# Performance work log

Measured on AMD Instinct MI355X. Metric: run time of the kernel, lower is better.

## Reference

```python
import jax, jax.numpy as jnp
import numpy as np

D = 64            # node_out_feats
G = 1000          # number of graphs in batch
NPG = 32          # nodes per graph
N = G * NPG       # total nodes = 32000
E = 80000         # total edges
NODE_IN = 74
EDGE_IN = 12
EH = 128          # edge_hidden_feats
STEPS_MP = 6
STEPS_S2S = 6
LSTM_LAYERS = 3
N_TASKS = 1


def setup_inputs() -> dict:
    key = jax.random.key(0)
    ks = jax.random.split(key, 32)

    def lin(k, fi, fo):
        return (jax.random.normal(k, (fi, fo), jnp.float32) / np.float32(np.sqrt(fi)))

    # edges constrained within graphs
    eg = jax.random.randint(ks[0], (E,), 0, G)
    inp = {
        "node_feats": jax.random.normal(ks[1], (N, NODE_IN), jnp.float32),
        "edge_feats": jax.random.normal(ks[2], (E, EDGE_IN), jnp.float32),
        "src": (eg * NPG + jax.random.randint(ks[3], (E,), 0, NPG)).astype(jnp.int32),
        "dst": (eg * NPG + jax.random.randint(ks[4], (E,), 0, NPG)).astype(jnp.int32),
        "segment_ids": (jnp.arange(N, dtype=jnp.int32) // NPG),
        "Wp": lin(ks[5], NODE_IN, D), "bp": jnp.zeros((D,), jnp.float32),
        "We1": lin(ks[6], EDGE_IN, EH), "be1": jnp.zeros((EH,), jnp.float32),
        "We2": lin(ks[7], EH, D * D), "be2": jnp.zeros((D * D,), jnp.float32),
        "b_conv": jnp.zeros((D,), jnp.float32),
        "gru_Wx": lin(ks[8], D, 3 * D), "gru_Wh": lin(ks[9], D, 3 * D),
        "gru_bx": jnp.zeros((3 * D,), jnp.float32), "gru_bh": jnp.zeros((3 * D,), jnp.float32),
        "Wout1": lin(ks[10], 2 * D, D), "bout1": jnp.zeros((D,), jnp.float32),
        "Wout2": lin(ks[11], D, N_TASKS), "bout2": jnp.zeros((N_TASKS,), jnp.float32),
    }
    for l in range(LSTM_LAYERS):
        fi = 2 * D if l == 0 else D
        inp[f"lstm_Wx{l}"] = lin(ks[12 + 4 * l], fi, 4 * D)
        inp[f"lstm_Wh{l}"] = lin(ks[13 + 4 * l], D, 4 * D)
        inp[f"lstm_bx{l}"] = jnp.zeros((4 * D,), jnp.float32)
        inp[f"lstm_bh{l}"] = jnp.zeros((4 * D,), jnp.float32)
    return inp


def reference(node_feats, edge_feats, src, dst, segment_ids,
              Wp, bp, We1, be1, We2, be2, b_conv,
              gru_Wx, gru_Wh, gru_bx, gru_bh,
              Wout1, bout1, Wout2, bout2,
              lstm_Wx0, lstm_Wh0, lstm_bx0, lstm_bh0,
              lstm_Wx1, lstm_Wh1, lstm_bx1, lstm_bh1,
              lstm_Wx2, lstm_Wh2, lstm_bx2, lstm_bh2):
    # ---- MPNNGNN ----
    h = jax.nn.relu(node_feats @ Wp + bp)                 # [N, D]
    hidden = h                                            # GRU hidden state
    # edge network -> per-edge [D, D] weight matrix (edge feats are constant,
    # so compute once; DGL recomputes each step with identical result)
    W_edge = (jax.nn.relu(edge_feats @ We1 + be1) @ We2 + be2).reshape(E, D, D)
    for _ in range(STEPS_MP):
        msg = jnp.einsum('ed,edo->eo', h[src], W_edge)    # [E, D] per-edge matvec
        agg = jax.ops.segment_sum(msg, dst, num_segments=N) + b_conv
        x = jax.nn.relu(agg)
        # GRU cell (torch gate order r, z, n)
        gx = x @ gru_Wx + gru_bx
        gh = hidden @ gru_Wh + gru_bh
        r = jax.nn.sigmoid(gx[:, :D] + gh[:, :D])
        z = jax.nn.sigmoid(gx[:, D:2 * D] + gh[:, D:2 * D])
        n = jnp.tanh(gx[:, 2 * D:] + r * gh[:, 2 * D:])
        hidden = (1.0 - z) * n + z * hidden
        h = hidden
    # ---- Set2Set readout ----
    lstm = [(lstm_Wx0, lstm_Wh0, lstm_bx0, lstm_bh0),
            (lstm_Wx1, lstm_Wh1, lstm_bx1, lstm_bh1),
            (lstm_Wx2, lstm_Wh2, lstm_bx2, lstm_bh2)]
    hs = [jnp.zeros((G, D), h.dtype) for _ in range(LSTM_LAYERS)]
    cs = [jnp.zeros((G, D), h.dtype) for _ in range(LSTM_LAYERS)]
    q_star = jnp.zeros((G, 2 * D), h.dtype)
    for _ in range(STEPS_S2S):
        xq = q_star
        for l, (Wx, Wh, bx, bh) in enumerate(lstm):
            gates = xq @ Wx + bx + hs[l] @ Wh + bh        # [G, 4D], torch order i,f,g,o
            i, f, g_, o = jnp.split(gates, 4, axis=-1)
            c = jax.nn.sigmoid(f) * cs[l] + jax.nn.sigmoid(i) * jnp.tanh(g_)
            hs[l] = jax.nn.sigmoid(o) * jnp.tanh(c)
            cs[l] = c
            xq = hs[l]
        q = xq                                            # [G, D]
        e = jnp.sum(h * q[segment_ids], axis=-1)          # [N] attention logits
        emax = jax.ops.segment_max(e, segment_ids, num_segments=G)
        ee = jnp.exp(e - emax[segment_ids])
        alpha = ee / jax.ops.segment_sum(ee, segment_ids, num_segments=G)[segment_ids]
        readout = jax.ops.segment_sum(h * alpha[:, None], segment_ids, num_segments=G)
        q_star = jnp.concatenate([q, readout], axis=-1)   # [G, 2D]
    # ---- prediction head ----
    pred = jax.nn.relu(q_star @ Wout1 + bout1) @ Wout2 + bout2
    return pred, q_star
```

## Files before the change

kernel.cpp:

```cpp
#include <hip/hip_runtime.h>

typedef __attribute__((ext_vector_type(8))) _Float16 f16x8;
typedef __attribute__((ext_vector_type(2))) _Float16 f16x2;
typedef __attribute__((ext_vector_type(4))) float floatx4;

union HFrag { uint4 u4; f16x8 v; unsigned short s[8]; };
union HS { _Float16 h; unsigned short u; };
union UH2 { unsigned int u; f16x2 h; };

__device__ __forceinline__ float bf2f(unsigned short u) {
  return __uint_as_float(((unsigned int)u) << 16);
}
__device__ __forceinline__ float h2f(unsigned short u) { HS z; z.u = u; return (float)z.h; }
__device__ __forceinline__ unsigned short f2h(float f) { HS z; z.h = (_Float16)f; return z.u; }
__device__ __forceinline__ float sigmf(float x) { return 1.0f / (1.0f + expf(-x)); }

__device__ __forceinline__ float ldi(const void* p, long i, bool f32) {
  return f32 ? ((const float*)p)[i] : bf2f(((const unsigned short*)p)[i]);
}

__device__ __forceinline__ void dma16(unsigned short* lds, const unsigned short* g) {
  __builtin_amdgcn_global_load_lds(
      (const __attribute__((address_space(1))) unsigned int*)g,
      (__attribute__((address_space(3))) unsigned int*)lds,
      16, 0, 0);
}

#define WAIT_VM4()   __builtin_amdgcn_s_waitcnt(0x0F74)
#define WAIT_VM0()   __builtin_amdgcn_s_waitcnt(0x0F70)
#define WAIT_LGKM0() __builtin_amdgcn_s_waitcnt(0xC07F)

#define SAFE_BARRIER() do {                      \
  __builtin_amdgcn_sched_barrier(0);             \
  WAIT_LGKM0();                                  \
  __builtin_amdgcn_s_barrier();                  \
  __builtin_amdgcn_sched_barrier(0);             \
} while (0)

#define NNODES 32000
#define NEDGES 80000
#define NGRAPH 1000

#define MFMA_F16 __builtin_amdgcn_mfma_f32_16x16x32_f16

__global__ __launch_bounds__(256) void detect_kernel(
    const unsigned short* __restrict__ nf, int* __restrict__ flag) {
  __shared__ float sm[256];
  float m = 0.f;
  for (int i = threadIdx.x; i < 4096; i += 256) {
    float v = fabsf(bf2f(nf[i]));
    if (isfinite(v)) m = fmaxf(m, v);
    else m = 1e30f;
  }
  sm[threadIdx.x] = m;
  __syncthreads();
  if (threadIdx.x == 0) {
    float mm = 0.f;
    for (int i = 0; i < 256; ++i) mm = fmaxf(mm, sm[i]);
    flag[0] = (mm > 1e6f) ? 1 : 0;
  }
}

__global__ __launch_bounds__(256) void prep_kernel(
    const int* __restrict__ dflag,
    const void* __restrict__ Wx, const void* __restrict__ Wh,
    const void* __restrict__ bx, const void* __restrict__ bh,
    const void* __restrict__ bconv,
    unsigned short* __restrict__ WxH, unsigned short* __restrict__ WhH,
    float* __restrict__ bxf, float* __restrict__ bhf, float* __restrict__ bconvf) {
  bool f32 = dflag[0] != 0;
  int idx = blockIdx.x * 256 + threadIdx.x;
  int j = idx >> 6, k = idx & 63;
  WxH[idx] = f2h(ldi(Wx, k * 192 + j, f32));
  WhH[idx] = f2h(ldi(Wh, k * 192 + j, f32));
  if (idx < 192) { bxf[idx] = ldi(bx, idx, f32); bhf[idx] = ldi(bh, idx, f32); }
  if (idx < 64) bconvf[idx] = ldi(bconv, idx, f32);
}

__global__ __launch_bounds__(256) void lstmprep_kernel(
    const int* __restrict__ dflag,
    const void* Wx0, const void* Wh0, const void* bx0, const void* bh0,
    const void* Wx1, const void* Wh1, const void* bx1, const void* bh1,
    const void* Wx2, const void* Wh2, const void* bx2, const void* bh2,
    float4* __restrict__ LW, float* __restrict__ bsum) {
  bool f32 = dflag[0] != 0;
  int idx = blockIdx.x * 256 + threadIdx.x;
  int l, base, fi;
  if (idx < 12288)      { l = 0; base = 0;     fi = 128; }
  else if (idx < 20480) { l = 1; base = 12288; fi = 64; }
  else                  { l = 2; base = 20480; fi = 64; }
  const void* Wx = (l == 0) ? Wx0 : (l == 1) ? Wx1 : Wx2;
  const void* Wh = (l == 0) ? Wh0 : (l == 1) ? Wh1 : Wh2;
  int r = idx - base;
  int c = r >> 8, t = r & 255;
  float v[4];
#pragma unroll
  for (int i2 = 0; i2 < 4; ++i2) {
    int k = c * 4 + i2;
    v[i2] = (k < fi) ? ldi(Wx, (long)k * 256 + t, f32)
                     : ldi(Wh, (long)(k - fi) * 256 + t, f32);
  }
  float4 o; o.x = v[0]; o.y = v[1]; o.z = v[2]; o.w = v[3];
  LW[idx] = o;
  if (idx < 768) {
    int ll = idx >> 8, j = idx & 255;
    const void* bx = (ll == 0) ? bx0 : (ll == 1) ? bx1 : bx2;
    const void* bh = (ll == 0) ? bh0 : (ll == 1) ? bh1 : bh2;
    bsum[idx] = ldi(bx, j, f32) + ldi(bh, j, f32);
  }
}

__global__ __launch_bounds__(256) void nodeproj_kernel(
    const int* __restrict__ dflag,
    const void* __restrict__ nf, const void* __restrict__ Wp,
    const void* __restrict__ bp, float* __restrict__ hstate) {
  bool f32 = dflag[0] != 0;
  int lane = threadIdx.x & 63;
  int n = blockIdx.x * 4 + (threadIdx.x >> 6);
  float acc = ldi(bp, lane, f32);
  for (int k = 0; k < 74; ++k)
    acc += ldi(nf, (long)n * 74 + k, f32) * ldi(Wp, k * 64 + lane, f32);
  hstate[n * 64 + lane] = fmaxf(acc, 0.0f);
}

__global__ __launch_bounds__(256) void we2t_kernel(
    const int* __restrict__ dflag,
    const void* __restrict__ We2, unsigned short* __restrict__ We2T) {
  bool f32 = dflag[0] != 0;
  int idx = blockIdx.x * 256 + threadIdx.x;
  int j = idx & 7;
  int gs = (idx >> 3) & 7;
  int o = (idx >> 6) & 63;
  int k = idx >> 12;
  int g = gs ^ (o & 7);
  int d = g * 8 + j;
  We2T[idx] = f2h(ldi(We2, (long)k * 4096 + d * 64 + o, f32));
}

__global__ __launch_bounds__(256) void be2t_kernel(
    const int* __restrict__ dflag,
    const void* __restrict__ be2, unsigned short* __restrict__ be2T) {
  bool f32 = dflag[0] != 0;
  int idx = blockIdx.x * 256 + threadIdx.x;
  int j = idx & 7;
  int gs = (idx >> 3) & 7;
  int o = idx >> 6;
  int g = gs ^ (o & 7);
  int d = g * 8 + j;
  be2T[idx] = f2h(ldi(be2, (long)d * 64 + o, f32));
}

__global__ __launch_bounds__(256) void count_kernel(
    const int* __restrict__ dst, int* __restrict__ cnt) {
  int e = blockIdx.x * 256 + threadIdx.x;
  if (e < NEDGES) atomicAdd(&cnt[dst[e]], 1);
}

__global__ __launch_bounds__(256) void scan_kernel(
    const int* __restrict__ cnt, int* __restrict__ row_ptr, int* __restrict__ cur) {
  __shared__ int part[256];
  int t = threadIdx.x;
  int base = t * 125;
  int s = 0;
  for (int i = 0; i < 125; ++i) s += cnt[base + i];
  part[t] = s;
  __syncthreads();
  if (t == 0) {
    int run = 0;
    for (int i = 0; i < 256; ++i) { int v = part[i]; part[i] = run; run += v; }
  }
  __syncthreads();
  int run = part[t];
  for (int i = 0; i < 125; ++i) {
    row_ptr[base + i] = run;
    cur[base + i] = run;
    run += cnt[base + i];
  }
  if (t == 255) row_ptr[32000] = run;
}

__global__ __launch_bounds__(256) void fill_kernel(
    const int* __restrict__ dst, int* __restrict__ cur, int* __restrict__ eidx) {
  int e = blockIdx.x * 256 + threadIdx.x;
  if (e < NEDGES) { int p = atomicAdd(&cur[dst[e]], 1); eidx[p] = e; }
}

__global__ __launch_bounds__(256, 2) void msg_z_kernel(
    const int* __restrict__ dflag,
    const float* __restrict__ hstate,
    const void* __restrict__ ef, const void* __restrict__ We1,
    const void* __restrict__ be1,
    const unsigned short* __restrict__ We2T,
    const unsigned short* __restrict__ be2T,
    const int* __restrict__ src, const int* __restrict__ eidx,
    const int* __restrict__ row_ptr,
    float* __restrict__ msgbuf) {
  bool f32 = dflag[0] != 0;
  __shared__ __align__(16) unsigned short BtL[2][8192];
  __shared__ __align__(16) unsigned int Zs[2][64][68];
  __shared__ float we1T_s[1536];
  __shared__ float be1_s[128];

  int t = threadIdx.x, lane = t & 63, w = t >> 6;
  int c16 = lane & 15, q = lane >> 4;
  int nb = blockIdx.x * 64;
  int p0 = row_ptr[nb], p1 = row_ptr[nb + 64];
  int nE = p1 - p0;
  if (nE <= 0) return;

  for (int i = t; i < 1536; i += 256) {
    int k = i / 12, j = i - k * 12;
    we1T_s[i] = ldi(We1, j * 128 + k, f32);
  }
  if (t < 128) be1_s[t] = ldi(be1, t, f32);

  HFrag bhi[4][2], blo[4][2];
#pragma unroll
  for (int nt = 0; nt < 4; ++nt)
#pragma unroll
    for (int ks = 0; ks < 2; ++ks) {
      const float* hp = hstate + (size_t)(nb + nt * 16 + c16) * 64 + ks * 32 + q * 8;
      float4 v0 = *(const float4*)hp;
      float4 v1 = *(const float4*)(hp + 4);
      float vv[8] = {v0.x, v0.y, v0.z, v0.w, v1.x, v1.y, v1.z, v1.w};
#pragma unroll
      for (int j = 0; j < 8; ++j) {
        HS hi; hi.h = (_Float16)vv[j];
        bhi[nt][ks].s[j] = hi.u;
        blo[nt][ks].s[j] = f2h(vv[j] - (float)hi.h);
      }
    }
  __syncthreads();

  int arow = (w * 16 + c16) * 64;
  int g0q = (q ^ (c16 & 7)) * 8;
  int g1q = ((4 + q) ^ (c16 & 7)) * 8;

  for (int et = 0; et < nE; et += 256) {
    if (et > 0) SAFE_BARRIER();
    int me = et + t;
    bool act = me < nE;
    int pos = p0 + (act ? me : 0);
    int eg = eidx[pos];
    int r = src[eg] - nb;
    float efr[12];
#pragma unroll
    for (int j = 0; j < 12; ++j) efr[j] = ldi(ef, (long)eg * 12 + j, f32);

    dma16(&BtL[0][0] + w * 1024, be2T + w * 1024 + lane * 8);
    dma16(&BtL[0][0] + w * 1024 + 512, be2T + w * 1024 + 512 + lane * 8);
    dma16(&BtL[1][0] + w * 1024, We2T + w * 1024 + lane * 8);
    dma16(&BtL[1][0] + w * 1024 + 512, We2T + w * 1024 + 512 + lane * 8);
    dma16(&BtL[1][0] + 4096 + w * 1024, We2T + 4096 + w * 1024 + lane * 8);
    dma16(&BtL[1][0] + 4096 + w * 1024 + 512, We2T + 4096 + w * 1024 + 512 + lane * 8);
    WAIT_VM0();

    floatx4 hacc[4];
#pragma unroll
    for (int nt = 0; nt < 4; ++nt) hacc[nt] = (floatx4){0.f, 0.f, 0.f, 0.f};
    {
      HFrag aB0, aB1;
      aB0.u4 = *(const uint4*)&BtL[0][arow + g0q];
      aB1.u4 = *(const uint4*)&BtL[0][arow + g1q];
#pragma unroll
      for (int nt = 0; nt < 4; ++nt) {
        hacc[nt] = MFMA_F16(aB0.v, bhi[nt][0].v, hacc[nt], 0, 0, 0);
        hacc[nt] = MFMA_F16(aB0.v, blo[nt][0].v, hacc[nt], 0, 0, 0);
        hacc[nt] = MFMA_F16(aB1.v, bhi[nt][1].v, hacc[nt], 0, 0, 0);
        hacc[nt] = MFMA_F16(aB1.v, blo[nt][1].v, hacc[nt], 0, 0, 0);
      }
    }
    __builtin_amdgcn_sched_barrier(0);
    WAIT_LGKM0();
    __builtin_amdgcn_sched_barrier(0);
    dma16(&BtL[0][0] + w * 1024, We2T + 8192 + w * 1024 + lane * 8);
    dma16(&BtL[0][0] + w * 1024 + 512, We2T + 8192 + w * 1024 + 512 + lane * 8);
    dma16(&BtL[0][0] + 4096 + w * 1024, We2T + 12288 + w * 1024 + lane * 8);
    dma16(&BtL[0][0] + 4096 + w * 1024 + 512, We2T + 12288 + w * 1024 + 512 + lane * 8);
#pragma unroll
    for (int nt = 0; nt < 4; ++nt)
      *(floatx4*)&Zs[1][nt * 16 + c16][w * 16 + q * 4] = hacc[nt];
    SAFE_BARRIER();

    floatx4 msgv[16];
    if (act) {
#pragma unroll
      for (int og = 0; og < 16; ++og)
        msgv[og] = *(const floatx4*)&Zs[1][r][og * 4];
    }

    for (int c = 0; c < 64; ++c) {
      int cb = (c + 1) & 1;
      int zc = c & 1;
      if (c == 63) WAIT_VM0(); else WAIT_VM4();
      HFrag a00, a01, a10, a11;
      a00.u4 = *(const uint4*)&BtL[cb][arow + g0q];
      a01.u4 = *(const uint4*)&BtL[cb][arow + g1q];
      a10.u4 = *(const uint4*)&BtL[cb][4096 + arow + g0q];
      a11.u4 = *(const uint4*)&BtL[cb][4096 + arow + g1q];
      __builtin_amdgcn_sched_barrier(0);
      WAIT_LGKM0();
      __builtin_amdgcn_sched_barrier(0);
      if (c + 2 < 64) {
        const unsigned short* G = We2T + (size_t)(c + 2) * 8192 + w * 1024 + lane * 8;
        unsigned short* L = &BtL[cb][0] + w * 1024;
        dma16(L, G); dma16(L + 512, G + 512);
        dma16(L + 4096, G + 4096); dma16(L + 4096 + 512, G + 4096 + 512);
      }
      floatx4 z0[4], z1[4];
#pragma unroll
      for (int nt = 0; nt < 4; ++nt) {
        z0[nt] = (floatx4){0.f, 0.f, 0.f, 0.f};
        z1[nt] = (floatx4){0.f, 0.f, 0.f, 0.f};
      }
#pragma unroll
      for (int nt = 0; nt < 4; ++nt) {
        z0[nt] = MFMA_F16(a00.v, bhi[nt][0].v, z0[nt], 0, 0, 0);
        z0[nt] = MFMA_F16(a00.v, blo[nt][0].v, z0[nt], 0, 0, 0);
        z0[nt] = MFMA_F16(a01.v, bhi[nt][1].v, z0[nt], 0, 0, 0);
        z0[nt] = MFMA_F16(a01.v, blo[nt][1].v, z0[nt], 0, 0, 0);
        z1[nt] = MFMA_F16(a10.v, bhi[nt][0].v, z1[nt], 0, 0, 0);
        z1[nt] = MFMA_F16(a10.v, blo[nt][0].v, z1[nt], 0, 0, 0);
        z1[nt] = MFMA_F16(a11.v, bhi[nt][1].v, z1[nt], 0, 0, 0);
        z1[nt] = MFMA_F16(a11.v, blo[nt][1].v, z1[nt], 0, 0, 0);
      }
#pragma unroll
      for (int nt = 0; nt < 4; ++nt) {
        uint4 st;
        HS p0h, p1h;
        p0h.h = (_Float16)z0[nt][0]; p1h.h = (_Float16)z1[nt][0];
        st.x = (unsigned int)p0h.u | ((unsigned int)p1h.u << 16);
        p0h.h = (_Float16)z0[nt][1]; p1h.h = (_Float16)z1[nt][1];
        st.y = (unsigned int)p0h.u | ((unsigned int)p1h.u << 16);
        p0h.h = (_Float16)z0[nt][2]; p1h.h = (_Float16)z1[nt][2];
        st.z = (unsigned int)p0h.u | ((unsigned int)p1h.u << 16);
        p0h.h = (_Float16)z0[nt][3]; p1h.h = (_Float16)z1[nt][3];
        st.w = (unsigned int)p0h.u | ((unsigned int)p1h.u << 16);
        *(uint4*)&Zs[zc][nt * 16 + c16][w * 16 + q * 4] = st;
      }
      SAFE_BARRIER();

      if (act) {
        int k0 = c * 2;
        float u0 = be1_s[k0], u1 = be1_s[k0 + 1];
#pragma unroll
        for (int j = 0; j < 12; ++j) {
          u0 += efr[j] * we1T_s[k0 * 12 + j];
          u1 += efr[j] * we1T_s[(k0 + 1) * 12 + j];
        }
        u0 = fmaxf(u0, 0.f); u1 = fmaxf(u1, 0.f);
        HS ua, ub; ua.h = (_Float16)u0; ub.h = (_Float16)u1;
        UH2 uu; uu.u = (unsigned int)ua.u | ((unsigned int)ub.u << 16);
#pragma unroll
        for (int og = 0; og < 16; ++og) {
          uint4 zz = *(const uint4*)&Zs[zc][r][og * 4];
          UH2 a;
          a.u = zz.x; msgv[og][0] = __builtin_amdgcn_fdot2(a.h, uu.h, msgv[og][0], false);
          a.u = zz.y; msgv[og][1] = __builtin_amdgcn_fdot2(a.h, uu.h, msgv[og][1], false);
          a.u = zz.z; msgv[og][2] = __builtin_amdgcn_fdot2(a.h, uu.h, msgv[og][2], false);
          a.u = zz.w; msgv[og][3] = __builtin_amdgcn_fdot2(a.h, uu.h, msgv[og][3], false);
        }
      }
    }

    if (act) {
      float* mp = msgbuf + (size_t)pos * 64;
#pragma unroll
      for (int og = 0; og < 16; ++og) *(floatx4*)(mp + og * 4) = msgv[og];
    }
  }
}

__global__ __launch_bounds__(256, 2) void gru_kernel(
    float* __restrict__ hstate, const float* __restrict__ msgbuf,
    const int* __restrict__ row_ptr,
    const unsigned short* __restrict__ WxH, const unsigned short* __restrict__ WhH,
    const float* __restrict__ bxf, const float* __restrict__ bhf,
    const float* __restrict__ bconvf) {
  __shared__ __align__(16) unsigned short Xhi[64][72];
  __shared__ __align__(16) unsigned short Xlo[64][72];
  __shared__ __align__(16) unsigned short Hh[64][72];
  __shared__ unsigned short SRZ[128][68];
  __shared__ float GXn[64][66];
  __shared__ float GHn[64][66];
  int t = threadIdx.x;
  int nb = blockIdx.x * 64;

#pragma unroll
  for (int i = 0; i < 16; ++i) {
    int idx = t + i * 256;
    int n = idx >> 6, c = idx & 63;
    int node = nb + n;
    float a = bconvf[c];
    int p0 = row_ptr[node], p1 = row_ptr[node + 1];
    for (int p = p0; p < p1; ++p) a += msgbuf[(size_t)p * 64 + c];
    a = fmaxf(a, 0.f);
    HS hi; hi.h = (_Float16)a;
    Xhi[n][c] = hi.u;
    Xlo[n][c] = f2h(a - (float)hi.h);
    Hh[n][c] = f2h(hstate[(size_t)node * 64 + c]);
  }
  __syncthreads();

  int lane = t & 63, w = t >> 6;
  int c16 = lane & 15, q = lane >> 4;
  floatx4 gx[3][4], gh[3][4];
#pragma unroll
  for (int jt = 0; jt < 3; ++jt)
#pragma unroll
    for (int nt = 0; nt < 4; ++nt) {
      gx[jt][nt] = (floatx4){0.f, 0.f, 0.f, 0.f};
      gh[jt][nt] = (floatx4){0.f, 0.f, 0.f, 0.f};
    }
#pragma unroll
  for (int kc = 0; kc < 2; ++kc) {
    int kof = kc * 32 + q * 8;
    HFrag ax[3], ah[3];
#pragma unroll
    for (int jt = 0; jt < 3; ++jt) {
      long off = (long)((w * 3 + jt) * 16 + c16) * 64 + kof;
      ax[jt].u4 = *(const uint4*)(WxH + off);
      ah[jt].u4 = *(const uint4*)(WhH + off);
    }
    HFrag bxh[4], bxl[4], bhf_[4];
#pragma unroll
    for (int nt = 0; nt < 4; ++nt) {
      int n = nt * 16 + c16;
      bxh[nt].u4 = *(const uint4*)&Xhi[n][kof];
      bxl[nt].u4 = *(const uint4*)&Xlo[n][kof];
      bhf_[nt].u4 = *(const uint4*)&Hh[n][kof];
    }
#pragma unroll
    for (int jt = 0; jt < 3; ++jt)
#pragma unroll
      for (int nt = 0; nt < 4; ++nt) {
        gx[jt][nt] = MFMA_F16(ax[jt].v, bxh[nt].v, gx[jt][nt], 0, 0, 0);
        gx[jt][nt] = MFMA_F16(ax[jt].v, bxl[nt].v, gx[jt][nt], 0, 0, 0);
        gh[jt][nt] = MFMA_F16(ah[jt].v, bhf_[nt].v, gh[jt][nt], 0, 0, 0);
      }
  }

#pragma unroll
  for (int jt = 0; jt < 3; ++jt) {
#pragma unroll
    for (int rr = 0; rr < 4; ++rr) {
      int j = (w * 3 + jt) * 16 + q * 4 + rr;
      float bxv = bxf[j], bhv = bhf[j];
#pragma unroll
      for (int nt = 0; nt < 4; ++nt) {
        int n = nt * 16 + c16;
        float vx = gx[jt][nt][rr] + bxv;
        float vh = gh[jt][nt][rr] + bhv;
        if (j < 128) {
          SRZ[j][n] = f2h(sigmf(vx + vh));
        } else {
          GXn[j - 128][n] = vx;
          GHn[j - 128][n] = vh;
        }
      }
    }
  }
  __syncthreads();

#pragma unroll
  for (int i = 0; i < 16; ++i) {
    int idx = t + i * 256;
    int n = idx >> 6, f = idx & 63;
    float r = h2f(SRZ[f][n]);
    float z = h2f(SRZ[64 + f][n]);
    float ng = tanhf(GXn[f][n] + r * GHn[f][n]);
    size_t gi = (size_t)(nb + n) * 64 + f;
    float ho = hstate[gi];
    hstate[gi] = (1.0f - z) * ng + z * ho;
  }
}

__global__ __launch_bounds__(512) void s2s6_kernel(
    const int* __restrict__ dflag,
    const float* __restrict__ hstate,
    const float4* __restrict__ LW,
    const float* __restrict__ lstm_bsum,
    const void* __restrict__ Wout1, const void* __restrict__ bout1,
    const void* __restrict__ Wout2, const void* __restrict__ bout2,
    float* __restrict__ out) {
  bool f32 = dflag[0] != 0;
  __shared__ float xq[4][128];
  __shared__ float inb[4][192];
  __shared__ float gates[4][256];
  __shared__ float al[4][32];
  __shared__ float hsvf[768];
  __shared__ float csvf[768];
  int g0 = blockIdx.x * 4;
  int t = threadIdx.x;

  for (int i = t; i < 512; i += 512) xq[i >> 7][i & 127] = 0.f;
  for (int i = t; i < 768; i += 512) { hsvf[i] = 0.f; csvf[i] = 0.f; }
  __syncthreads();

  int tt = t & 255, gp = t >> 8;
  int ga = gp * 2, gb = ga + 1;

  for (int s = 0; s < 6; ++s) {
#pragma unroll
    for (int l = 0; l < 3; ++l) {
      const int fi = (l == 0) ? 128 : 64;
      const int tot = fi + 64;
      for (int i = t; i < 4 * tot; i += 512) {
        int g = i / tot, k = i - g * tot;
        inb[g][k] = (k < fi) ? xq[g][k] : hsvf[l * 256 + g * 64 + (k - fi)];
      }
      __syncthreads();
      const int nch = tot >> 2;
      const float4* wrow = LW + ((l == 0) ? 0 : (l == 1) ? 12288 : 20480) + tt;
      float bs = lstm_bsum[l * 256 + tt];
      float a0 = bs, a1 = bs;
#pragma unroll 8
      for (int cch = 0; cch < nch; ++cch) {
        float4 wv = wrow[(size_t)cch * 256];
        float4 x0 = *(const float4*)&inb[ga][cch * 4];
        float4 x1 = *(const float4*)&inb[gb][cch * 4];
        a0 += wv.x * x0.x + wv.y * x0.y + wv.z * x0.z + wv.w * x0.w;
        a1 += wv.x * x1.x + wv.y * x1.y + wv.z * x1.z + wv.w * x1.w;
      }
      gates[ga][tt] = a0;
      gates[gb][tt] = a1;
      __syncthreads();
      if (t < 256) {
        int gg = t >> 6, u = t & 63;
        float ig = sigmf(gates[gg][u]);
        float fg = sigmf(gates[gg][64 + u]);
        float gv = tanhf(gates[gg][128 + u]);
        float og = sigmf(gates[gg][192 + u]);
        int ci = l * 256 + t;
        float cc = fg * csvf[ci] + ig * gv;
        float hn = og * tanhf(cc);
        csvf[ci] = cc;
        hsvf[ci] = hn;
        xq[gg][u] = hn;
      }
      __syncthreads();
    }
    if (t < 256) {
      int gg = t >> 6, tl = t & 63;
      int g = g0 + gg;
      int n = tl & 31, half = tl >> 5;
      const float* hrow = hstate + (size_t)(g * 32 + n) * 64 + half * 32;
      const float* qp = &xq[gg][half * 32];
      float p = 0.f;
#pragma unroll
      for (int k = 0; k < 32; ++k) p += hrow[k] * qp[k];
      p += __shfl_xor(p, 32, 64);
      if (half == 0) {
        float m = p;
#pragma unroll
        for (int s2 = 1; s2 < 32; s2 <<= 1) m = fmaxf(m, __shfl_xor(m, s2, 32));
        float e = expf(p - m);
        float sum = e;
#pragma unroll
        for (int s2 = 1; s2 < 32; s2 <<= 1) sum += __shfl_xor(sum, s2, 32);
        al[gg][n] = e / sum;
      }
      float acc = 0.f;
#pragma unroll 8
      for (int nn = 0; nn < 32; ++nn)
        acc += al[gg][nn] * hstate[(size_t)(g * 32 + nn) * 64 + tl];
      xq[gg][64 + tl] = acc;
    }
    __syncthreads();
  }

  if (t < 256) {
    int gg = t >> 6, tl = t & 63;
    int g = g0 + gg;
    float acc = ldi(bout1, tl, f32);
#pragma unroll 16
    for (int k = 0; k < 128; ++k) acc += xq[gg][k] * ldi(Wout1, k * 64 + tl, f32);
    acc = fmaxf(acc, 0.0f);
    float p = acc * ldi(Wout2, tl, f32);
#pragma unroll
    for (int m = 1; m < 64; m <<= 1) p += __shfl_xor(p, m, 64);
    if (tl == 0) out[g] = p + ldi(bout2, 0, f32);
    out[1000 + g * 128 + tl] = xq[gg][tl];
    out[1000 + g * 128 + 64 + tl] = xq[gg][64 + tl];
  }
}

extern "C" void kernel_launch(void* const* d_in, const int* in_sizes, int n_in,
                              void* d_out, int out_size, void* d_ws, size_t ws_size,
                              hipStream_t stream) {
  (void)in_sizes; (void)n_in; (void)out_size; (void)ws_size;
  const void* node_feats = d_in[0];
  const void* edge_feats = d_in[1];
  const int* src = (const int*)d_in[2];
  const int* dst = (const int*)d_in[3];
  const void* Wp = d_in[5];
  const void* bp = d_in[6];
  const void* We1 = d_in[7];
  const void* be1 = d_in[8];
  const void* We2 = d_in[9];
  const void* be2 = d_in[10];
  const void* b_conv = d_in[11];
  const void* gWx = d_in[12];
  const void* gWh = d_in[13];
  const void* gbx = d_in[14];
  const void* gbh = d_in[15];
  const void* Wout1 = d_in[16];
  const void* bout1 = d_in[17];
  const void* Wout2 = d_in[18];
  const void* bout2 = d_in[19];

  int* dflag = (int*)d_ws;
  float* hstate = (float*)d_ws + 64;
  float* msgbuf = hstate + NNODES * 64;
  unsigned short* We2T = (unsigned short*)(msgbuf + (size_t)NEDGES * 64);
  unsigned short* WxH = We2T + 524288;
  unsigned short* WhH = WxH + 12288;
  float* bxf = (float*)(WhH + 12288);
  float* bhf = bxf + 192;
  float* bconvf = bhf + 192;
  int* row_ptr = (int*)(bconvf + 64);
  int* cur = row_ptr + 32001;
  int* cnt = cur + 32000;
  int* eidx = cnt + 32000;
  uintptr_t lwp = (uintptr_t)(eidx + 80000);
  lwp = (lwp + 15) & ~(uintptr_t)15;
  float4* LWf = (float4*)lwp;
  float* lstm_bsum = (float*)(LWf + 28672);
  unsigned short* be2T = (unsigned short*)(lstm_bsum + 768);

  (void)hipMemsetAsync(cnt, 0, (size_t)NNODES * sizeof(int), stream);

  detect_kernel<<<1, 256, 0, stream>>>((const unsigned short*)node_feats, dflag);
  prep_kernel<<<48, 256, 0, stream>>>(dflag, gWx, gWh, gbx, gbh, b_conv,
                                      WxH, WhH, bxf, bhf, bconvf);
  nodeproj_kernel<<<NNODES / 4, 256, 0, stream>>>(dflag, node_feats, Wp, bp, hstate);
  we2t_kernel<<<2048, 256, 0, stream>>>(dflag, We2, We2T);
  be2t_kernel<<<16, 256, 0, stream>>>(dflag, be2, be2T);
  lstmprep_kernel<<<112, 256, 0, stream>>>(dflag,
      d_in[20], d_in[21], d_in[22], d_in[23],
      d_in[24], d_in[25], d_in[26], d_in[27],
      d_in[28], d_in[29], d_in[30], d_in[31],
      LWf, lstm_bsum);

  count_kernel<<<(NEDGES + 255) / 256, 256, 0, stream>>>(dst, cnt);
  scan_kernel<<<1, 256, 0, stream>>>(cnt, row_ptr, cur);
  fill_kernel<<<(NEDGES + 255) / 256, 256, 0, stream>>>(dst, cur, eidx);

  for (int step = 0; step < 6; ++step) {
    msg_z_kernel<<<NNODES / 64, 256, 0, stream>>>(
        dflag, hstate, edge_feats, We1, be1, We2T, be2T, src, eidx, row_ptr,
        msgbuf);
    gru_kernel<<<NNODES / 64, 256, 0, stream>>>(hstate, msgbuf, row_ptr,
                                                WxH, WhH, bxf, bhf, bconvf);
  }
  s2s6_kernel<<<NGRAPH / 4, 512, 0, stream>>>(dflag, hstate,
      (const float4*)LWf, lstm_bsum,
      Wout1, bout1, Wout2, bout2, (float*)d_out);
}
```

Baseline: 1.181 ms.

## Fuse message and GRU kernels and precompute edge hidden features once

Adds an uprep kernel that computes the ReLU edge hidden vectors once, packed as fp16 pairs, since they do not change across the six message-passing steps. Merges the message kernel and the GRU kernel into a single step kernel, so each block sums its messages in LDS instead of writing and re-reading a per-edge message buffer in global memory. The GRU's h operand now reuses the already-split hstate fragments, and the chunk loop is unrolled by two. The cost is more LDS per block through aliased buffers, an extra per-chunk global load of the precomputed u values, and extra barriers for the in-LDS aggregation.

```diff
diff --git a/kernel.cpp b/kernel.cpp
--- a/kernel.cpp
+++ b/kernel.cpp
@@ -26,7 +26,7 @@
       16, 0, 0);
 }
 
-#define WAIT_VM4()   __builtin_amdgcn_s_waitcnt(0x0F74)
+#define WAIT_VM5()   __builtin_amdgcn_s_waitcnt(0x0F75)
 #define WAIT_VM0()   __builtin_amdgcn_s_waitcnt(0x0F70)
 #define WAIT_LGKM0() __builtin_amdgcn_s_waitcnt(0xC07F)
 
@@ -185,34 +185,119 @@
   if (e < NEDGES) { int p = atomicAdd(&cur[dst[e]], 1); eidx[p] = e; }
 }
 
-__global__ __launch_bounds__(256, 2) void msg_z_kernel(
+__global__ __launch_bounds__(256) void uprep_kernel(
     const int* __restrict__ dflag,
-    const float* __restrict__ hstate,
     const void* __restrict__ ef, const void* __restrict__ We1,
-    const void* __restrict__ be1,
+    const void* __restrict__ be1, const int* __restrict__ eidx,
+    unsigned int* __restrict__ uT) {
+  bool f32 = dflag[0] != 0;
+  int kp = blockIdx.y;
+  int pos = blockIdx.x * 256 + threadIdx.x;
+  if (pos >= NEDGES) return;
+  int e = eidx[pos];
+  int k0 = kp * 2;
+  float u0 = ldi(be1, k0, f32), u1 = ldi(be1, k0 + 1, f32);
+#pragma unroll
+  for (int j = 0; j < 12; ++j) {
+    float efv = ldi(ef, (long)e * 12 + j, f32);
+    u0 += efv * ldi(We1, j * 128 + k0, f32);
+    u1 += efv * ldi(We1, j * 128 + k0 + 1, f32);
+  }
+  u0 = fmaxf(u0, 0.f); u1 = fmaxf(u1, 0.f);
+  HS a, b; a.h = (_Float16)u0; b.h = (_Float16)u1;
+  uT[(size_t)kp * NEDGES + pos] = (unsigned int)a.u | ((unsigned int)b.u << 16);
+}
+
+__device__ __forceinline__ void issueB(unsigned short* L, const unsigned short* G,
+                                       int w, int lane) {
+  L += w * 1024; G += w * 1024 + lane * 8;
+  dma16(L, G); dma16(L + 512, G + 512);
+  dma16(L + 4096, G + 4096); dma16(L + 4096 + 512, G + 4096 + 512);
+}
+
+__device__ __forceinline__ void zchunk(
+    unsigned short (*BtL)[8192], unsigned int (*Zs)[64][68],
+    const HFrag (&bhi)[4][2], const HFrag (&blo)[4][2],
+    int arow, int g0q, int g1q, int c16, int w, int q,
+    int cb, int zc, bool act, int r, unsigned int ucur, floatx4 (&msgv)[16]) {
+  HFrag a00, a01, a10, a11;
+  a00.u4 = *(const uint4*)&BtL[cb][arow + g0q];
+  a01.u4 = *(const uint4*)&BtL[cb][arow + g1q];
+  a10.u4 = *(const uint4*)&BtL[cb][4096 + arow + g0q];
+  a11.u4 = *(const uint4*)&BtL[cb][4096 + arow + g1q];
+  __builtin_amdgcn_sched_barrier(0);
+  WAIT_LGKM0();
+  __builtin_amdgcn_sched_barrier(0);
+  floatx4 z0[4], z1[4];
+#pragma unroll
+  for (int nt = 0; nt < 4; ++nt) {
+    z0[nt] = (floatx4){0.f, 0.f, 0.f, 0.f};
+    z1[nt] = (floatx4){0.f, 0.f, 0.f, 0.f};
+  }
+#pragma unroll
+  for (int nt = 0; nt < 4; ++nt) {
+    z0[nt] = MFMA_F16(a00.v, bhi[nt][0].v, z0[nt], 0, 0, 0);
+    z0[nt] = MFMA_F16(a00.v, blo[nt][0].v, z0[nt], 0, 0, 0);
+    z0[nt] = MFMA_F16(a01.v, bhi[nt][1].v, z0[nt], 0, 0, 0);
+    z0[nt] = MFMA_F16(a01.v, blo[nt][1].v, z0[nt], 0, 0, 0);
+    z1[nt] = MFMA_F16(a10.v, bhi[nt][0].v, z1[nt], 0, 0, 0);
+    z1[nt] = MFMA_F16(a10.v, blo[nt][0].v, z1[nt], 0, 0, 0);
+    z1[nt] = MFMA_F16(a11.v, bhi[nt][1].v, z1[nt], 0, 0, 0);
+    z1[nt] = MFMA_F16(a11.v, blo[nt][1].v, z1[nt], 0, 0, 0);
+  }
+#pragma unroll
+  for (int nt = 0; nt < 4; ++nt) {
+    uint4 st;
+    HS p0h, p1h;
+    p0h.h = (_Float16)z0[nt][0]; p1h.h = (_Float16)z1[nt][0];
+    st.x = (unsigned int)p0h.u | ((unsigned int)p1h.u << 16);
+    p0h.h = (_Float16)z0[nt][1]; p1h.h = (_Float16)z1[nt][1];
+    st.y = (unsigned int)p0h.u | ((unsigned int)p1h.u << 16);
+    p0h.h = (_Float16)z0[nt][2]; p1h.h = (_Float16)z1[nt][2];
+    st.z = (unsigned int)p0h.u | ((unsigned int)p1h.u << 16);
+    p0h.h = (_Float16)z0[nt][3]; p1h.h = (_Float16)z1[nt][3];
+    st.w = (unsigned int)p0h.u | ((unsigned int)p1h.u << 16);
+    *(uint4*)&Zs[zc][nt * 16 + c16][w * 16 + q * 4] = st;
+  }
+  SAFE_BARRIER();
+  if (act) {
+    UH2 uu; uu.u = ucur;
+#pragma unroll
+    for (int og = 0; og < 16; ++og) {
+      uint4 zz = *(const uint4*)&Zs[zc][r][og * 4];
+      UH2 a;
+      a.u = zz.x; msgv[og][0] = __builtin_amdgcn_fdot2(a.h, uu.h, msgv[og][0], false);
+      a.u = zz.y; msgv[og][1] = __builtin_amdgcn_fdot2(a.h, uu.h, msgv[og][1], false);
+      a.u = zz.z; msgv[og][2] = __builtin_amdgcn_fdot2(a.h, uu.h, msgv[og][2], false);
+      a.u = zz.w; msgv[og][3] = __builtin_amdgcn_fdot2(a.h, uu.h, msgv[og][3], false);
+    }
+  }
+}
+
+__global__ __launch_bounds__(256, 2) void step_fused_kernel(
     const unsigned short* __restrict__ We2T,
     const unsigned short* __restrict__ be2T,
+    const unsigned int* __restrict__ uT,
     const int* __restrict__ src, const int* __restrict__ eidx,
     const int* __restrict__ row_ptr,
-    float* __restrict__ msgbuf) {
-  bool f32 = dflag[0] != 0;
-  __shared__ __align__(16) unsigned short BtL[2][8192];
-  __shared__ __align__(16) unsigned int Zs[2][64][68];
-  __shared__ float we1T_s[1536];
-  __shared__ float be1_s[128];
+    const unsigned short* __restrict__ WxH, const unsigned short* __restrict__ WhH,
+    const float* __restrict__ bxf, const float* __restrict__ bhf,
+    const float* __restrict__ bconvf,
+    float* __restrict__ hstate) {
+  __shared__ __align__(16) unsigned char RA[67584];
+  unsigned short (*BtL)[8192] = (unsigned short (*)[8192])RA;
+  unsigned int (*Zs)[64][68] = (unsigned int (*)[64][68])(RA + 32768);
+  float (*MS)[64] = (float (*)[64])RA;
+  unsigned short (*Xhi)[72] = (unsigned short (*)[72])RA;
+  unsigned short (*Xlo)[72] = (unsigned short (*)[72])(RA + 9216);
+  unsigned short (*SRZ)[65] = (unsigned short (*)[65])(RA + 18432);
+  float (*NG)[65] = (float (*)[65])(RA + 35072);
 
   int t = threadIdx.x, lane = t & 63, w = t >> 6;
   int c16 = lane & 15, q = lane >> 4;
   int nb = blockIdx.x * 64;
   int p0 = row_ptr[nb], p1 = row_ptr[nb + 64];
   int nE = p1 - p0;
-  if (nE <= 0) return;
-
-  for (int i = t; i < 1536; i += 256) {
-    int k = i / 12, j = i - k * 12;
-    we1T_s[i] = ldi(We1, j * 128 + k, f32);
-  }
-  if (t < 128) be1_s[t] = ldi(be1, t, f32);
 
   HFrag bhi[4][2], blo[4][2];
 #pragma unroll
@@ -230,29 +315,28 @@
         blo[nt][ks].s[j] = f2h(vv[j] - (float)hi.h);
       }
     }
-  __syncthreads();
 
   int arow = (w * 16 + c16) * 64;
   int g0q = (q ^ (c16 & 7)) * 8;
   int g1q = ((4 + q) ^ (c16 & 7)) * 8;
 
+  float aggv[16];
+  {
+    float bcv = bconvf[lane];
+#pragma unroll
+    for (int i = 0; i < 16; ++i) aggv[i] = bcv;
+  }
+
   for (int et = 0; et < nE; et += 256) {
-    if (et > 0) SAFE_BARRIER();
     int me = et + t;
     bool act = me < nE;
     int pos = p0 + (act ? me : 0);
-    int eg = eidx[pos];
-    int r = src[eg] - nb;
-    float efr[12];
-#pragma unroll
-    for (int j = 0; j < 12; ++j) efr[j] = ldi(ef, (long)eg * 12 + j, f32);
-
+    int r = src[eidx[pos]] - nb;
+
+    unsigned int uA = uT[pos];
     dma16(&BtL[0][0] + w * 1024, be2T + w * 1024 + lane * 8);
     dma16(&BtL[0][0] + w * 1024 + 512, be2T + w * 1024 + 512 + lane * 8);
-    dma16(&BtL[1][0] + w * 1024, We2T + w * 1024 + lane * 8);
-    dma16(&BtL[1][0] + w * 1024 + 512, We2T + w * 1024 + 512 + lane * 8);
-    dma16(&BtL[1][0] + 4096 + w * 1024, We2T + 4096 + w * 1024 + lane * 8);
-    dma16(&BtL[1][0] + 4096 + w * 1024 + 512, We2T + 4096 + w * 1024 + 512 + lane * 8);
+    issueB(&BtL[1][0], We2T, w, lane);
     WAIT_VM0();
 
     floatx4 hacc[4];
@@ -273,10 +357,8 @@
     __builtin_amdgcn_sched_barrier(0);
     WAIT_LGKM0();
     __builtin_amdgcn_sched_barrier(0);
-    dma16(&BtL[0][0] + w * 1024, We2T + 8192 + w * 1024 + lane * 8);
-    dma16(&BtL[0][0] + w * 1024 + 512, We2T + 8192 + w * 1024 + 512 + lane * 8);
-    dma16(&BtL[0][0] + 4096 + w * 1024, We2T + 12288 + w * 1024 + lane * 8);
-    dma16(&BtL[0][0] + 4096 + w * 1024 + 512, We2T + 12288 + w * 1024 + 512 + lane * 8);
+    unsigned int uB = uT[(size_t)NEDGES + pos];
+    issueB(&BtL[0][0], We2T + 8192, w, lane);
 #pragma unroll
     for (int nt = 0; nt < 4; ++nt)
       *(floatx4*)&Zs[1][nt * 16 + c16][w * 16 + q * 4] = hacc[nt];
@@ -289,121 +371,63 @@
         msgv[og] = *(const floatx4*)&Zs[1][r][og * 4];
     }
 
-    for (int c = 0; c < 64; ++c) {
-      int cb = (c + 1) & 1;
-      int zc = c & 1;
-      if (c == 63) WAIT_VM0(); else WAIT_VM4();
-      HFrag a00, a01, a10, a11;
-      a00.u4 = *(const uint4*)&BtL[cb][arow + g0q];
-      a01.u4 = *(const uint4*)&BtL[cb][arow + g1q];
-      a10.u4 = *(const uint4*)&BtL[cb][4096 + arow + g0q];
-      a11.u4 = *(const uint4*)&BtL[cb][4096 + arow + g1q];
-      __builtin_amdgcn_sched_barrier(0);
-      WAIT_LGKM0();
-      __builtin_amdgcn_sched_barrier(0);
-      if (c + 2 < 64) {
-        const unsigned short* G = We2T + (size_t)(c + 2) * 8192 + w * 1024 + lane * 8;
-        unsigned short* L = &BtL[cb][0] + w * 1024;
-        dma16(L, G); dma16(L + 512, G + 512);
-        dma16(L + 4096, G + 4096); dma16(L + 4096 + 512, G + 4096 + 512);
-      }
-      floatx4 z0[4], z1[4];
-#pragma unroll
-      for (int nt = 0; nt < 4; ++nt) {
-        z0[nt] = (floatx4){0.f, 0.f, 0.f, 0.f};
-        z1[nt] = (floatx4){0.f, 0.f, 0.f, 0.f};
-      }
-#pragma unroll
-      for (int nt = 0; nt < 4; ++nt) {
-        z0[nt] = MFMA_F16(a00.v, bhi[nt][0].v, z0[nt], 0, 0, 0);
-        z0[nt] = MFMA_F16(a00.v, blo[nt][0].v, z0[nt], 0, 0, 0);
-        z0[nt] = MFMA_F16(a01.v, bhi[nt][1].v, z0[nt], 0, 0, 0);
-        z0[nt] = MFMA_F16(a01.v, blo[nt][1].v, z0[nt], 0, 0, 0);
-        z1[nt] = MFMA_F16(a10.v, bhi[nt][0].v, z1[nt], 0, 0, 0);
-        z1[nt] = MFMA_F16(a10.v, blo[nt][0].v, z1[nt], 0, 0, 0);
-        z1[nt] = MFMA_F16(a11.v, bhi[nt][1].v, z1[nt], 0, 0, 0);
-        z1[nt] = MFMA_F16(a11.v, blo[nt][1].v, z1[nt], 0, 0, 0);
-      }
-#pragma unroll
-      for (int nt = 0; nt < 4; ++nt) {
-        uint4 st;
-        HS p0h, p1h;
-        p0h.h = (_Float16)z0[nt][0]; p1h.h = (_Float16)z1[nt][0];
-        st.x = (unsigned int)p0h.u | ((unsigned int)p1h.u << 16);
-        p0h.h = (_Float16)z0[nt][1]; p1h.h = (_Float16)z1[nt][1];
-        st.y = (unsigned int)p0h.u | ((unsigned int)p1h.u << 16);
-        p0h.h = (_Float16)z0[nt][2]; p1h.h = (_Float16)z1[nt][2];
-        st.z = (unsigned int)p0h.u | ((unsigned int)p1h.u << 16);
-        p0h.h = (_Float16)z0[nt][3]; p1h.h = (_Float16)z1[nt][3];
-        st.w = (unsigned int)p0h.u | ((unsigned int)p1h.u << 16);
-        *(uint4*)&Zs[zc][nt * 16 + c16][w * 16 + q * 4] = st;
-      }
-      SAFE_BARRIER();
-
-      if (act) {
-        int k0 = c * 2;
-        float u0 = be1_s[k0], u1 = be1_s[k0 + 1];
-#pragma unroll
-        for (int j = 0; j < 12; ++j) {
-          u0 += efr[j] * we1T_s[k0 * 12 + j];
-          u1 += efr[j] * we1T_s[(k0 + 1) * 12 + j];
-        }
-        u0 = fmaxf(u0, 0.f); u1 = fmaxf(u1, 0.f);
-        HS ua, ub; ua.h = (_Float16)u0; ub.h = (_Float16)u1;
-        UH2 uu; uu.u = (unsigned int)ua.u | ((unsigned int)ub.u << 16);
-#pragma unroll
-        for (int og = 0; og < 16; ++og) {
-          uint4 zz = *(const uint4*)&Zs[zc][r][og * 4];
-          UH2 a;
-          a.u = zz.x; msgv[og][0] = __builtin_amdgcn_fdot2(a.h, uu.h, msgv[og][0], false);
-          a.u = zz.y; msgv[og][1] = __builtin_amdgcn_fdot2(a.h, uu.h, msgv[og][1], false);
-          a.u = zz.z; msgv[og][2] = __builtin_amdgcn_fdot2(a.h, uu.h, msgv[og][2], false);
-          a.u = zz.w; msgv[og][3] = __builtin_amdgcn_fdot2(a.h, uu.h, msgv[og][3], false);
-        }
-      }
-    }
-
+    for (int cc = 0; cc < 32; ++cc) {
+      const int c0 = cc * 2;
+      WAIT_VM5();
+      zchunk(BtL, Zs, bhi, blo, arow, g0q, g1q, c16, w, q, 1, 0, act, r, uA, msgv);
+      if (c0 + 2 < 64) {
+        __builtin_amdgcn_sched_barrier(0);
+        uA = uT[(size_t)(c0 + 2) * NEDGES + pos];
+        issueB(&BtL[1][0], We2T + (size_t)(c0 + 2) * 8192, w, lane);
+      }
+      if (c0 + 1 == 63) WAIT_VM0(); else WAIT_VM5();
+      zchunk(BtL, Zs, bhi, blo, arow, g0q, g1q, c16, w, q, 0, 1, act, r, uB, msgv);
+      if (c0 + 3 < 64) {
+        __builtin_amdgcn_sched_barrier(0);
+        uB = uT[(size_t)(c0 + 3) * NEDGES + pos];
+        issueB(&BtL[0][0], We2T + (size_t)(c0 + 3) * 8192, w, lane);
+      }
+    }
+
+    __syncthreads();
     if (act) {
-      float* mp = msgbuf + (size_t)pos * 64;
-#pragma unroll
-      for (int og = 0; og < 16; ++og) *(floatx4*)(mp + og * 4) = msgv[og];
-    }
-  }
-}
-
-__global__ __launch_bounds__(256, 2) void gru_kernel(
-    float* __restrict__ hstate, const float* __restrict__ msgbuf,
-    const int* __restrict__ row_ptr,
-    const unsigned short* __restrict__ WxH, const unsigned short* __restrict__ WhH,
-    const float* __restrict__ bxf, const float* __restrict__ bhf,
-    const float* __restrict__ bconvf) {
-  __shared__ __align__(16) unsigned short Xhi[64][72];
-  __shared__ __align__(16) unsigned short Xlo[64][72];
-  __shared__ __align__(16) unsigned short Hh[64][72];
-  __shared__ unsigned short SRZ[128][68];
-  __shared__ float GXn[64][66];
-  __shared__ float GHn[64][66];
-  int t = threadIdx.x;
-  int nb = blockIdx.x * 64;
+      int t7 = t & 7;
+#pragma unroll
+      for (int og = 0; og < 16; ++og)
+        *(floatx4*)&MS[t][(og ^ t7) * 4] = msgv[og];
+    }
+    __syncthreads();
+    {
+      int nT = nE - et; if (nT > 256) nT = 256;
+      int c = t & 63;
+      int cq = c >> 2, cj = c & 3;
+#pragma unroll
+      for (int i = 0; i < 16; ++i) {
+        int node = nb + (t >> 6) + i * 4;
+        int rs = row_ptr[node] - p0 - et;
+        int re = row_ptr[node + 1] - p0 - et;
+        int lo = rs < 0 ? 0 : rs;
+        int hi = re > nT ? nT : re;
+        float a = aggv[i];
+        for (int p = lo; p < hi; ++p)
+          a += MS[p][((cq ^ (p & 7)) << 2) | cj];
+        aggv[i] = a;
+      }
+    }
+    __syncthreads();
+  }
 
 #pragma unroll
   for (int i = 0; i < 16; ++i) {
-    int idx = t + i * 256;
-    int n = idx >> 6, c = idx & 63;
-    int node = nb + n;
-    float a = bconvf[c];
-    int p0 = row_ptr[node], p1 = row_ptr[node + 1];
-    for (int p = p0; p < p1; ++p) a += msgbuf[(size_t)p * 64 + c];
-    a = fmaxf(a, 0.f);
-    HS hi; hi.h = (_Float16)a;
-    Xhi[n][c] = hi.u;
-    Xlo[n][c] = f2h(a - (float)hi.h);
-    Hh[n][c] = f2h(hstate[(size_t)node * 64 + c]);
+    int n = (t >> 6) + i * 4;
+    int c = t & 63;
+    float x = fmaxf(aggv[i], 0.f);
+    HS hx; hx.h = (_Float16)x;
+    Xhi[n][c] = hx.u;
+    Xlo[n][c] = f2h(x - (float)hx.h);
   }
   __syncthreads();
 
-  int lane = t & 63, w = t >> 6;
-  int c16 = lane & 15, q = lane >> 4;
   floatx4 gx[3][4], gh[3][4];
 #pragma unroll
   for (int jt = 0; jt < 3; ++jt)
@@ -422,13 +446,12 @@
       ax[jt].u4 = *(const uint4*)(WxH + off);
       ah[jt].u4 = *(const uint4*)(WhH + off);
     }
-    HFrag bxh[4], bxl[4], bhf_[4];
+    HFrag bxh[4], bxl[4];
 #pragma unroll
     for (int nt = 0; nt < 4; ++nt) {
       int n = nt * 16 + c16;
       bxh[nt].u4 = *(const uint4*)&Xhi[n][kof];
       bxl[nt].u4 = *(const uint4*)&Xlo[n][kof];
-      bhf_[nt].u4 = *(const uint4*)&Hh[n][kof];
     }
 #pragma unroll
     for (int jt = 0; jt < 3; ++jt)
@@ -436,7 +459,7 @@
       for (int nt = 0; nt < 4; ++nt) {
         gx[jt][nt] = MFMA_F16(ax[jt].v, bxh[nt].v, gx[jt][nt], 0, 0, 0);
         gx[jt][nt] = MFMA_F16(ax[jt].v, bxl[nt].v, gx[jt][nt], 0, 0, 0);
-        gh[jt][nt] = MFMA_F16(ah[jt].v, bhf_[nt].v, gh[jt][nt], 0, 0, 0);
+        gh[jt][nt] = MFMA_F16(ah[jt].v, bhi[nt][kc].v, gh[jt][nt], 0, 0, 0);
       }
   }
 
@@ -448,14 +471,13 @@
       float bxv = bxf[j], bhv = bhf[j];
 #pragma unroll
       for (int nt = 0; nt < 4; ++nt) {
-        int n = nt * 16 + c16;
         float vx = gx[jt][nt][rr] + bxv;
         float vh = gh[jt][nt][rr] + bhv;
         if (j < 128) {
-          SRZ[j][n] = f2h(sigmf(vx + vh));
+          SRZ[j][nt * 16 + c16] = f2h(sigmf(vx + vh));
         } else {
-          GXn[j - 128][n] = vx;
-          GHn[j - 128][n] = vh;
+          gx[jt][nt][rr] = vx;
+          gh[jt][nt][rr] = vh;
         }
       }
     }
@@ -463,12 +485,29 @@
   __syncthreads();
 
 #pragma unroll
+  for (int jt = 0; jt < 3; ++jt) {
+#pragma unroll
+    for (int rr = 0; rr < 4; ++rr) {
+      int j = (w * 3 + jt) * 16 + q * 4 + rr;
+      if (j >= 128) {
+        int f = j - 128;
+#pragma unroll
+        for (int nt = 0; nt < 4; ++nt) {
+          int n = nt * 16 + c16;
+          float rg = h2f(SRZ[f][n]);
+          NG[f][n] = tanhf(gx[jt][nt][rr] + rg * gh[jt][nt][rr]);
+        }
+      }
+    }
+  }
+  __syncthreads();
+
+#pragma unroll
   for (int i = 0; i < 16; ++i) {
-    int idx = t + i * 256;
-    int n = idx >> 6, f = idx & 63;
-    float r = h2f(SRZ[f][n]);
+    int n = (t >> 6) + i * 4;
+    int f = t & 63;
     float z = h2f(SRZ[64 + f][n]);
-    float ng = tanhf(GXn[f][n] + r * GHn[f][n]);
+    float ng = NG[f][n];
     size_t gi = (size_t)(nb + n) * 64 + f;
     float ho = hstate[gi];
     hstate[gi] = (1.0f - z) * ng + z * ho;
@@ -611,8 +650,8 @@
 
   int* dflag = (int*)d_ws;
   float* hstate = (float*)d_ws + 64;
-  float* msgbuf = hstate + NNODES * 64;
-  unsigned short* We2T = (unsigned short*)(msgbuf + (size_t)NEDGES * 64);
+  unsigned int* uT = (unsigned int*)(hstate + NNODES * 64);
+  unsigned short* We2T = (unsigned short*)(uT + (size_t)NEDGES * 64);
   unsigned short* WxH = We2T + 524288;
   unsigned short* WhH = WxH + 12288;
   float* bxf = (float*)(WhH + 12288);
@@ -645,13 +684,14 @@
   count_kernel<<<(NEDGES + 255) / 256, 256, 0, stream>>>(dst, cnt);
   scan_kernel<<<1, 256, 0, stream>>>(cnt, row_ptr, cur);
   fill_kernel<<<(NEDGES + 255) / 256, 256, 0, stream>>>(dst, cur, eidx);
+  {
+    dim3 ug((NEDGES + 255) / 256, 64);
+    uprep_kernel<<<ug, 256, 0, stream>>>(dflag, edge_feats, We1, be1, eidx, uT);
+  }
 
   for (int step = 0; step < 6; ++step) {
-    msg_z_kernel<<<NNODES / 64, 256, 0, stream>>>(
-        dflag, hstate, edge_feats, We1, be1, We2T, be2T, src, eidx, row_ptr,
-        msgbuf);
-    gru_kernel<<<NNODES / 64, 256, 0, stream>>>(hstate, msgbuf, row_ptr,
-                                                WxH, WhH, bxf, bhf, bconvf);
+    step_fused_kernel<<<NNODES / 64, 256, 0, stream>>>(
+        We2T, be2T, uT, src, eidx, row_ptr, WxH, WhH, bxf, bhf, bconvf, hstate);
   }
   s2s6_kernel<<<NGRAPH / 4, 512, 0, stream>>>(dflag, hstate,
       (const float4*)LWf, lstm_bsum,
```

After: 1.265 ms. 7.1% more time.
